# Kernel optimization log

Measured on AMD Instinct MI355X. Metric: run time of the kernel, lower is better.

Reference implementation:

```python
import jax, jax.numpy as jnp
import numpy as np

HIDDEN_DIM = 256
ATTN_DIM = 256
N_TOKENS = 32768
N_CODES = 4096
RMS_EPS = 1e-5


def _rms_norm(x, weight):
    # fp32 variance like the torch module, eps=1e-5, elementwise affine (no bias)
    var = jnp.mean(x.astype(jnp.float32) ** 2, axis=-1, keepdims=True)
    x = x * jax.lax.rsqrt(var + RMS_EPS)
    return x * weight


def setup_inputs() -> dict:
    key = jax.random.key(0)
    ks = jax.random.split(key, 10)
    s_in = 1.0 / np.sqrt(HIDDEN_DIM).astype(np.float32)
    return {
        "hidden_states": jax.random.normal(ks[0], (N_TOKENS, HIDDEN_DIM), jnp.float32),
        "codebook_hidden_states": jax.random.normal(ks[1], (N_CODES, HIDDEN_DIM), jnp.float32),
        # Linear weights stored as [in, out] (y = x @ W + b)
        "wq": jax.random.normal(ks[2], (HIDDEN_DIM, ATTN_DIM), jnp.float32) * s_in,
        "bq": jnp.zeros((ATTN_DIM,), jnp.float32),
        "wk": jax.random.normal(ks[3], (HIDDEN_DIM, ATTN_DIM), jnp.float32) * s_in,
        "bk": jnp.zeros((ATTN_DIM,), jnp.float32),
        "wv": jax.random.normal(ks[4], (HIDDEN_DIM, HIDDEN_DIM), jnp.float32) * s_in,
        "bv": jnp.zeros((HIDDEN_DIM,), jnp.float32),
        "gq": jnp.ones((ATTN_DIM,), jnp.float32),  # RMSNorm weight for q
        "gk": jnp.ones((ATTN_DIM,), jnp.float32),  # RMSNorm weight for k
    }


def reference(hidden_states, codebook_hidden_states, wq, bq, wk, bk, wv, bv, gq, gk):
    # projections (small-d GEMMs)
    q = hidden_states @ wq + bq                     # [NT, A]
    k = codebook_hidden_states @ wk + bk            # [N, A]
    v = codebook_hidden_states @ wv + bv            # [N, C]

    scale = 1.0 / jnp.sqrt(jnp.asarray(q.shape[-1], q.dtype))
    q = _rms_norm(q, gq)
    k = _rms_norm(k, gk)

    logits = jnp.einsum("bd,nd->bn", q, k) * scale  # [NT, N]
    soft_one_hot = jax.nn.softmax(logits, axis=1)
    idx_N = jnp.argmax(logits, axis=1)              # argmax(softmax) == argmax(logits)
    hard_one_hot = jax.nn.one_hot(idx_N, logits.shape[1], dtype=logits.dtype)
    # straight-through estimator
    one_hot = hard_one_hot - jax.lax.stop_gradient(soft_one_hot) + soft_one_hot

    z_q = jnp.einsum("bn,nd->bd", one_hot, v)       # [NT, C]
    z_q_2 = jnp.einsum("bn,nd->bd", hard_one_hot, v)
    return (logits, idx_N[:, None], z_q, z_q_2)
```

## Files before the change

kernel.cpp:

```cpp
#include <hip/hip_runtime.h>
#include <hip/hip_bf16.h>


#define NTOK 32768
#define NCODE 4096
#define DIM 256

typedef __bf16 bf16x8 __attribute__((ext_vector_type(8)));
typedef float f32x4 __attribute__((ext_vector_type(4)));

__device__ __forceinline__ void nt_store4(const float4& v, float* p) {
    f32x4 w; w[0] = v.x; w[1] = v.y; w[2] = v.z; w[3] = v.w;
    __builtin_nontemporal_store(w, (f32x4*)p);
}

__global__ __launch_bounds__(256, 2)
void gemm_fused(const float* __restrict__ hs, const float* __restrict__ cb,
                const float* __restrict__ wq, const float* __restrict__ bq,
                const float* __restrict__ wk, const float* __restrict__ bk,
                const float* __restrict__ wv, const float* __restrict__ bv,
                float* __restrict__ qf, float* __restrict__ kf, float* __restrict__ vf)
{
    __shared__ __align__(16) float Xs[32][132];
    __shared__ __align__(16) float Ws[32][132];
    const int t  = threadIdx.x;
    const int tm = t >> 4;
    const int tn = t & 15;

    const int bx = blockIdx.x;
    const float* X; const float* W; const float* bias; float* Y; int mb;
    if (bx < 32)      { X = cb; W = wk; bias = bk; Y = kf; mb = bx * 128; }
    else if (bx < 64) { X = cb; W = wv; bias = bv; Y = vf; mb = (bx - 32) * 128; }
    else              { X = hs; W = wq; bias = bq; Y = qf; mb = (bx - 64) * 128; }
    const int nb = blockIdx.y * 128;

    float acc[8][8];
    #pragma unroll
    for (int i = 0; i < 8; ++i)
        #pragma unroll
        for (int j = 0; j < 8; ++j) acc[i][j] = 0.f;

    const int sxm = t >> 1;
    const int sxh = (t & 1) * 16;
    const int swk = t >> 3;
    const int swc = (t & 7) * 16;

    for (int kb = 0; kb < 256; kb += 32) {
        float4 xv[4], wv4[4];
        #pragma unroll
        for (int i = 0; i < 4; ++i) {
            xv[i]  = *(const float4*)&X[(size_t)(mb + sxm) * 256 + kb + sxh + 4 * i];
            wv4[i] = *(const float4*)&W[(size_t)(kb + swk) * 256 + nb + swc + 4 * i];
        }
        __syncthreads();
        #pragma unroll
        for (int i = 0; i < 4; ++i) {
            Xs[sxh + 4*i + 0][sxm] = xv[i].x;
            Xs[sxh + 4*i + 1][sxm] = xv[i].y;
            Xs[sxh + 4*i + 2][sxm] = xv[i].z;
            Xs[sxh + 4*i + 3][sxm] = xv[i].w;
            *(float4*)&Ws[swk][swc + 4*i] = wv4[i];
        }
        __syncthreads();
        #pragma unroll 8
        for (int kk = 0; kk < 32; ++kk) {
            float4 a0 = *(const float4*)&Xs[kk][tm*8];
            float4 a1 = *(const float4*)&Xs[kk][tm*8 + 4];
            float4 b0 = *(const float4*)&Ws[kk][tn*8];
            float4 b1 = *(const float4*)&Ws[kk][tn*8 + 4];
            float av[8] = {a0.x,a0.y,a0.z,a0.w,a1.x,a1.y,a1.z,a1.w};
            float bw[8] = {b0.x,b0.y,b0.z,b0.w,b1.x,b1.y,b1.z,b1.w};
            #pragma unroll
            for (int i = 0; i < 8; ++i)
                #pragma unroll
                for (int j = 0; j < 8; ++j)
                    acc[i][j] = fmaf(av[i], bw[j], acc[i][j]);
        }
    }

    float4 bb0 = *(const float4*)&bias[nb + tn*8];
    float4 bb1 = *(const float4*)&bias[nb + tn*8 + 4];
    float bb[8] = {bb0.x,bb0.y,bb0.z,bb0.w,bb1.x,bb1.y,bb1.z,bb1.w};
    #pragma unroll
    for (int i = 0; i < 8; ++i) {
        const size_t row = (size_t)(mb + tm*8 + i);
        float4 o0 = {acc[i][0]+bb[0], acc[i][1]+bb[1], acc[i][2]+bb[2], acc[i][3]+bb[3]};
        float4 o1 = {acc[i][4]+bb[4], acc[i][5]+bb[5], acc[i][6]+bb[6], acc[i][7]+bb[7]};
        *(float4*)&Y[row*256 + nb + tn*8]     = o0;
        *(float4*)&Y[row*256 + nb + tn*8 + 4] = o1;
    }
}

__global__ __launch_bounds__(256)
void rmsnorm_fused(float* __restrict__ kf, float* __restrict__ qf,
                   const float* __restrict__ gk, const float* __restrict__ gq,
                   __hip_bfloat16* __restrict__ kb, __hip_bfloat16* __restrict__ qb)
{
    const int b = blockIdx.x;
    float* X; const float* g; __hip_bfloat16* Xb; size_t row;
    if (b < 1024) { X = kf; g = gk; Xb = kb; row = (size_t)b * 4 + (threadIdx.x >> 6); }
    else { X = qf; g = gq; Xb = qb; row = (size_t)(b - 1024) * 4 + (threadIdx.x >> 6); }

    const int lane = threadIdx.x & 63;
    float4 x = *(const float4*)&X[row*256 + lane*4];
    float ssq = fmaf(x.x, x.x, fmaf(x.y, x.y, fmaf(x.z, x.z, x.w * x.w)));
    #pragma unroll
    for (int o = 1; o < 64; o <<= 1) ssq += __shfl_xor(ssq, o, 64);
    const float r = 1.0f / sqrtf(ssq * (1.0f/256.0f) + 1e-5f);
    float4 gg = *(const float4*)&g[lane*4];
    float y0 = (x.x*r)*gg.x, y1 = (x.y*r)*gg.y, y2 = (x.z*r)*gg.z, y3 = (x.w*r)*gg.w;
    float4 y = {y0, y1, y2, y3};
    *(float4*)&X[row*256 + lane*4] = y;
    __hip_bfloat16 h0 = __float2bfloat16(y0), h1 = __float2bfloat16(y1);
    __hip_bfloat16 h2 = __float2bfloat16(y2), h3 = __float2bfloat16(y3);
    ushort4 p;
    p.x = *(unsigned short*)&h0; p.y = *(unsigned short*)&h1;
    p.z = *(unsigned short*)&h2; p.w = *(unsigned short*)&h3;
    ((ushort4*)Xb)[row*64 + lane] = p;
}

__device__ __forceinline__ void load_lds16(const void* g, void* l) {
    __builtin_amdgcn_global_load_lds((const __attribute__((address_space(1))) unsigned int*)g,
                                     (__attribute__((address_space(3))) unsigned int*)l, 16, 0, 0);
}

__global__ __launch_bounds__(256, 4)
void mfma_logits(const __hip_bfloat16* __restrict__ Qb, const __hip_bfloat16* __restrict__ Kb,
                 float* __restrict__ Out, float* __restrict__ Tmax)
{
    __shared__ __align__(16) char smem[33792];
    __hip_bfloat16* Asm = (__hip_bfloat16*)smem;
    __hip_bfloat16* Bsm = (__hip_bfloat16*)(smem + 16384);
    float*          Eps = (float*)smem;
    float*          Pmax = (float*)(smem + 32768);

    const int t    = threadIdx.x;
    const int lane = t & 63;
    const int w    = t >> 6;
    const int wm = w >> 1, wn = w & 1;

    const int bid = blockIdx.x;
    const int xcd = bid & 7;
    const int cid = bid >> 3;
    const int mb  = (xcd * 32 + (cid & 31)) * 128;
    const int ctl = cid >> 5;
    const int nb  = ctl * 128;

    const int grow   = t >> 3;
    const int gslot  = (t & 7) ^ ((t >> 3) & 7);
    const __hip_bfloat16* gA = Qb + (size_t)(mb + grow) * 256 + gslot * 8;
    const __hip_bfloat16* gB = Kb + (size_t)(nb + grow) * 256 + gslot * 8;
    __hip_bfloat16* lA = &Asm[w * 512];
    __hip_bfloat16* lB = &Bsm[w * 512];

    const int fr = lane & 15;
    const int kq = lane >> 4;
    const int rswz = lane & 7;
    const int ra0 = (wm * 64 + fr) * 64;
    const int rb0 = (wn * 64 + fr) * 64;

    f32x4 acc[4][4];
    #pragma unroll
    for (int mi = 0; mi < 4; ++mi)
        #pragma unroll
        for (int ni = 0; ni < 4; ++ni) {
            acc[mi][ni][0] = 0.f; acc[mi][ni][1] = 0.f;
            acc[mi][ni][2] = 0.f; acc[mi][ni][3] = 0.f;
        }

    for (int ks = 0; ks < 4; ++ks) {
        const int k0 = ks * 64;
        #pragma unroll
        for (int i = 0; i < 4; ++i) {
            load_lds16(gA + (size_t)i * 32 * 256 + k0, lA + i * 2048);
            load_lds16(gB + (size_t)i * 32 * 256 + k0, lB + i * 2048);
        }
        __syncthreads();

        #pragma unroll
        for (int kh = 0; kh < 2; ++kh) {
            bf16x8 af[4], bg[4];
            #pragma unroll
            for (int mi = 0; mi < 4; ++mi)
                af[mi] = *(const bf16x8*)&Asm[ra0 + mi*16*64 + (((kh<<2) + kq) ^ rswz) * 8];
            #pragma unroll
            for (int ni = 0; ni < 4; ++ni)
                bg[ni] = *(const bf16x8*)&Bsm[rb0 + ni*16*64 + (((kh<<2) + kq) ^ rswz) * 8];
            #pragma unroll
            for (int mi = 0; mi < 4; ++mi)
                #pragma unroll
                for (int ni = 0; ni < 4; ++ni)
                    acc[mi][ni] = __builtin_amdgcn_mfma_f32_16x16x32_bf16(
                        af[mi], bg[ni], acc[mi][ni], 0, 0, 0);
        }
        __syncthreads();
    }

    #pragma unroll
    for (int mi = 0; mi < 4; ++mi)
        #pragma unroll
        for (int j = 0; j < 4; ++j) {
            float mx = fmaxf(fmaxf(acc[mi][0][j], acc[mi][1][j]),
                             fmaxf(acc[mi][2][j], acc[mi][3][j]));
            #pragma unroll
            for (int o = 1; o < 16; o <<= 1) mx = fmaxf(mx, __shfl_xor(mx, o, 64));
            if ((lane & 15) == 0)
                Pmax[(wm*64 + mi*16 + (lane>>4)*4 + j)*2 + wn] = mx;
        }

    const int cr = (lane >> 4) * 4;
    const int cc = lane & 15;
    #pragma unroll
    for (int c = 0; c < 2; ++c) {
        if (wm == c) {
            #pragma unroll
            for (int mi = 0; mi < 4; ++mi)
                #pragma unroll
                for (int ni = 0; ni < 4; ++ni) {
                    const int lrow = mi*16 + cr;
                    const int lcol = wn*64 + ni*16 + cc;
                    #pragma unroll
                    for (int j = 0; j < 4; ++j) {
                        float v = acc[mi][ni][j] * 0.0625f;
                        v = fminf(fmaxf(v, -16.0f), 16.0f);
                        Eps[(lrow + j) * 128 + lcol] = v;
                    }
                }
        }
        __syncthreads();
        #pragma unroll
        for (int it = 0; it < 8; ++it) {
            const int p   = it * 1024 + t * 4;
            const int row = p >> 7;
            const int col = p & 127;
            float4 v = *(const float4*)&Eps[p];
            nt_store4(v, &Out[(size_t)(mb + c*64 + row) * 4096 + nb + col]);
        }
        __syncthreads();
    }

    if (t < 128) {
        float raw = fmaxf(Pmax[t*2], Pmax[t*2 + 1]);
        float v = raw * 0.0625f;
        v = fminf(fmaxf(v, -16.0f), 16.0f);
        Tmax[(size_t)(mb + t) * 32 + ctl] = v;
    }
}

__device__ __forceinline__ float dot256_f32(const float* __restrict__ a, const float* __restrict__ b)
{
    float s0 = 0.f, s1 = 0.f, s2 = 0.f, s3 = 0.f;
    #pragma unroll 8
    for (int j = 0; j < 64; ++j) {
        float4 x = ((const float4*)a)[j];
        float4 y = ((const float4*)b)[j];
        s0 = fmaf(x.x, y.x, s0);
        s1 = fmaf(x.y, y.y, s1);
        s2 = fmaf(x.z, y.z, s2);
        s3 = fmaf(x.w, y.w, s3);
    }
    return (s0 + s1) + (s2 + s3);
}

__global__ __launch_bounds__(256)
void refine_argmax_fast(const float* __restrict__ L, const float* __restrict__ Tmax,
                        const float* __restrict__ Qf, const float* __restrict__ Kf,
                        const float* __restrict__ Vf, float* __restrict__ OutIdx,
                        float* __restrict__ Zq, float* __restrict__ Zq2)
{
    __shared__ int cnt[4];
    __shared__ int list[4][256];
    const int lane = threadIdx.x & 63;
    const int w    = threadIdx.x >> 6;
    const size_t row = (size_t)blockIdx.x * 4 + w;

    float tm = (lane < 32) ? Tmax[row * 32 + lane] : -INFINITY;
    float gmax = tm;
    #pragma unroll
    for (int o = 1; o < 64; o <<= 1) gmax = fmaxf(gmax, __shfl_xor(gmax, o, 64));
    const float thr = gmax - 0.5f;

    if (lane == 0) cnt[w] = 0;
    __syncthreads();

    for (int tile = 0; tile < 32; ++tile) {
        const float tmt = __shfl(tm, tile, 64);
        if (tmt >= thr) {
            const float2 v2 = *(const float2*)&L[row * 4096 + tile * 128 + lane * 2];
            if (v2.x >= thr) {
                int slot = atomicAdd(&cnt[w], 1);
                if (slot < 256) list[w][slot] = tile*128 + lane*2;
            }
            if (v2.y >= thr) {
                int slot = atomicAdd(&cnt[w], 1);
                if (slot < 256) list[w][slot] = tile*128 + lane*2 + 1;
            }
        }
    }
    __syncthreads();

    int m = cnt[w]; if (m > 256) m = 256;
    float bv = -INFINITY;
    int   bi = 0x7fffffff;
    const float* qrow = Qf + row * 256;
    for (int base = 0; base < m; base += 64) {
        const int ci = base + lane;
        if (ci < m) {
            const int c = list[w][ci];
            float rv = dot256_f32(qrow, Kf + (size_t)c * 256) * 0.0625f;
            if (rv > bv || (rv == bv && c < bi)) { bv = rv; bi = c; }
        }
    }
    #pragma unroll
    for (int o = 1; o < 64; o <<= 1) {
        float ov = __shfl_xor(bv, o, 64);
        int   oi = __shfl_xor(bi, o, 64);
        if (ov > bv || (ov == bv && oi < bi)) { bv = ov; bi = oi; }
    }

    if (bi < 0) bi = 0;
    if (bi > 4095) bi = 4095;

    if (lane == 0) __builtin_nontemporal_store((float)bi, &OutIdx[row]);

    float4 vv = ((const float4*)(Vf + (size_t)bi * 256))[lane];
    nt_store4(vv, (float*)&((float4*)Zq)[row*64 + lane]);
    nt_store4(vv, (float*)&((float4*)Zq2)[row*64 + lane]);
}

extern "C" void kernel_launch(void* const* d_in, const int* in_sizes, int n_in,
                              void* d_out, int out_size, void* d_ws, size_t ws_size,
                              hipStream_t stream)
{
    (void)in_sizes; (void)n_in; (void)out_size;
    const float* hs = (const float*)d_in[0];
    const float* cb = (const float*)d_in[1];
    const float* wq = (const float*)d_in[2];
    const float* bq = (const float*)d_in[3];
    const float* wk = (const float*)d_in[4];
    const float* bk = (const float*)d_in[5];
    const float* wv = (const float*)d_in[6];
    const float* bv = (const float*)d_in[7];
    const float* gq = (const float*)d_in[8];
    const float* gk = (const float*)d_in[9];
    float* out = (float*)d_out;

    if (ws_size < 31457280u) return;

    float* qf = out + 134250496ull;

    char* ws = (char*)d_ws;
    float* kf = (float*)ws;
    float* vf = (float*)(ws + 4194304);
    __hip_bfloat16* qb = (__hip_bfloat16*)(ws + 8388608);
    __hip_bfloat16* kb = (__hip_bfloat16*)(ws + 25165824);
    float* tmax = (float*)(ws + 27262976);

    gemm_fused<<<dim3(320, 2), 256, 0, stream>>>(hs, cb, wq, bq, wk, bk, wv, bv,
                                                 qf, kf, vf);
    rmsnorm_fused<<<9216, 256, 0, stream>>>(kf, qf, gk, gq, kb, qb);
    mfma_logits<<<8192, 256, 0, stream>>>(qb, kb, out, tmax);
    refine_argmax_fast<<<8192, 256, 0, stream>>>(out, tmax, qf, kf, vf,
        out + 134217728ull,
        out + 134250496ull,
        out + 142639104ull);
}
```

Before: 441.3 us.

## Fuse RMSNorm into projection GEMM by computing full rows per block

```diff
diff --git a/kernel.cpp b/kernel.cpp
--- a/kernel.cpp
+++ b/kernel.cpp
@@ -15,11 +15,13 @@
 }
 
 __global__ __launch_bounds__(256, 2)
-void gemm_fused(const float* __restrict__ hs, const float* __restrict__ cb,
+void gemm3_norm(const float* __restrict__ hs, const float* __restrict__ cb,
                 const float* __restrict__ wq, const float* __restrict__ bq,
                 const float* __restrict__ wk, const float* __restrict__ bk,
                 const float* __restrict__ wv, const float* __restrict__ bv,
-                float* __restrict__ qf, float* __restrict__ kf, float* __restrict__ vf)
+                const float* __restrict__ gq, const float* __restrict__ gk,
+                float* __restrict__ qf, float* __restrict__ kf, float* __restrict__ vf,
+                __hip_bfloat16* __restrict__ qb16, __hip_bfloat16* __restrict__ kb16)
 {
     __shared__ __align__(16) float Xs[32][132];
     __shared__ __align__(16) float Ws[32][132];
@@ -29,94 +31,96 @@
 
     const int bx = blockIdx.x;
     const float* X; const float* W; const float* bias; float* Y; int mb;
-    if (bx < 32)      { X = cb; W = wk; bias = bk; Y = kf; mb = bx * 128; }
-    else if (bx < 64) { X = cb; W = wv; bias = bv; Y = vf; mb = (bx - 32) * 128; }
-    else              { X = hs; W = wq; bias = bq; Y = qf; mb = (bx - 64) * 128; }
-    const int nb = blockIdx.y * 128;
-
-    float acc[8][8];
-    #pragma unroll
-    for (int i = 0; i < 8; ++i)
-        #pragma unroll
-        for (int j = 0; j < 8; ++j) acc[i][j] = 0.f;
+    const float* g = nullptr; __hip_bfloat16* Yb = nullptr; bool donorm;
+    if (bx < 32)      { X = cb; W = wk; bias = bk; Y = kf; mb = bx * 128;        g = gk; Yb = kb16; donorm = true;  }
+    else if (bx < 64) { X = cb; W = wv; bias = bv; Y = vf; mb = (bx - 32) * 128; donorm = false; }
+    else              { X = hs; W = wq; bias = bq; Y = qf; mb = (bx - 64) * 128; g = gq; Yb = qb16; donorm = true;  }
 
     const int sxm = t >> 1;
     const int sxh = (t & 1) * 16;
     const int swk = t >> 3;
     const int swc = (t & 7) * 16;
 
-    for (int kb = 0; kb < 256; kb += 32) {
-        float4 xv[4], wv4[4];
-        #pragma unroll
-        for (int i = 0; i < 4; ++i) {
-            xv[i]  = *(const float4*)&X[(size_t)(mb + sxm) * 256 + kb + sxh + 4 * i];
-            wv4[i] = *(const float4*)&W[(size_t)(kb + swk) * 256 + nb + swc + 4 * i];
-        }
-        __syncthreads();
-        #pragma unroll
-        for (int i = 0; i < 4; ++i) {
-            Xs[sxh + 4*i + 0][sxm] = xv[i].x;
-            Xs[sxh + 4*i + 1][sxm] = xv[i].y;
-            Xs[sxh + 4*i + 2][sxm] = xv[i].z;
-            Xs[sxh + 4*i + 3][sxm] = xv[i].w;
-            *(float4*)&Ws[swk][swc + 4*i] = wv4[i];
-        }
-        __syncthreads();
-        #pragma unroll 8
-        for (int kk = 0; kk < 32; ++kk) {
-            float4 a0 = *(const float4*)&Xs[kk][tm*8];
-            float4 a1 = *(const float4*)&Xs[kk][tm*8 + 4];
-            float4 b0 = *(const float4*)&Ws[kk][tn*8];
-            float4 b1 = *(const float4*)&Ws[kk][tn*8 + 4];
-            float av[8] = {a0.x,a0.y,a0.z,a0.w,a1.x,a1.y,a1.z,a1.w};
-            float bw[8] = {b0.x,b0.y,b0.z,b0.w,b1.x,b1.y,b1.z,b1.w};
-            #pragma unroll
-            for (int i = 0; i < 8; ++i)
+    #pragma unroll 1
+    for (int h = 0; h < 2; ++h) {
+        const int nb = h * 128;
+
+        float acc[8][8];
+        #pragma unroll
+        for (int i = 0; i < 8; ++i)
+            #pragma unroll
+            for (int j = 0; j < 8; ++j) acc[i][j] = 0.f;
+
+        for (int kb = 0; kb < 256; kb += 32) {
+            float4 xv[4], wv4[4];
+            #pragma unroll
+            for (int i = 0; i < 4; ++i) {
+                xv[i]  = *(const float4*)&X[(size_t)(mb + sxm) * 256 + kb + sxh + 4 * i];
+                wv4[i] = *(const float4*)&W[(size_t)(kb + swk) * 256 + nb + swc + 4 * i];
+            }
+            __syncthreads();
+            #pragma unroll
+            for (int i = 0; i < 4; ++i) {
+                Xs[sxh + 4*i + 0][sxm] = xv[i].x;
+                Xs[sxh + 4*i + 1][sxm] = xv[i].y;
+                Xs[sxh + 4*i + 2][sxm] = xv[i].z;
+                Xs[sxh + 4*i + 3][sxm] = xv[i].w;
+                *(float4*)&Ws[swk][swc + 4*i] = wv4[i];
+            }
+            __syncthreads();
+            #pragma unroll 8
+            for (int kk = 0; kk < 32; ++kk) {
+                float4 a0 = *(const float4*)&Xs[kk][tm*8];
+                float4 a1 = *(const float4*)&Xs[kk][tm*8 + 4];
+                float4 b0 = *(const float4*)&Ws[kk][tn*8];
+                float4 b1 = *(const float4*)&Ws[kk][tn*8 + 4];
+                float av[8] = {a0.x,a0.y,a0.z,a0.w,a1.x,a1.y,a1.z,a1.w};
+                float bw[8] = {b0.x,b0.y,b0.z,b0.w,b1.x,b1.y,b1.z,b1.w};
                 #pragma unroll
-                for (int j = 0; j < 8; ++j)
-                    acc[i][j] = fmaf(av[i], bw[j], acc[i][j]);
-        }
-    }
-
-    float4 bb0 = *(const float4*)&bias[nb + tn*8];
-    float4 bb1 = *(const float4*)&bias[nb + tn*8 + 4];
-    float bb[8] = {bb0.x,bb0.y,bb0.z,bb0.w,bb1.x,bb1.y,bb1.z,bb1.w};
-    #pragma unroll
-    for (int i = 0; i < 8; ++i) {
-        const size_t row = (size_t)(mb + tm*8 + i);
-        float4 o0 = {acc[i][0]+bb[0], acc[i][1]+bb[1], acc[i][2]+bb[2], acc[i][3]+bb[3]};
-        float4 o1 = {acc[i][4]+bb[4], acc[i][5]+bb[5], acc[i][6]+bb[6], acc[i][7]+bb[7]};
-        *(float4*)&Y[row*256 + nb + tn*8]     = o0;
-        *(float4*)&Y[row*256 + nb + tn*8 + 4] = o1;
-    }
-}
-
-__global__ __launch_bounds__(256)
-void rmsnorm_fused(float* __restrict__ kf, float* __restrict__ qf,
-                   const float* __restrict__ gk, const float* __restrict__ gq,
-                   __hip_bfloat16* __restrict__ kb, __hip_bfloat16* __restrict__ qb)
-{
-    const int b = blockIdx.x;
-    float* X; const float* g; __hip_bfloat16* Xb; size_t row;
-    if (b < 1024) { X = kf; g = gk; Xb = kb; row = (size_t)b * 4 + (threadIdx.x >> 6); }
-    else { X = qf; g = gq; Xb = qb; row = (size_t)(b - 1024) * 4 + (threadIdx.x >> 6); }
-
-    const int lane = threadIdx.x & 63;
-    float4 x = *(const float4*)&X[row*256 + lane*4];
-    float ssq = fmaf(x.x, x.x, fmaf(x.y, x.y, fmaf(x.z, x.z, x.w * x.w)));
-    #pragma unroll
-    for (int o = 1; o < 64; o <<= 1) ssq += __shfl_xor(ssq, o, 64);
-    const float r = 1.0f / sqrtf(ssq * (1.0f/256.0f) + 1e-5f);
-    float4 gg = *(const float4*)&g[lane*4];
-    float y0 = (x.x*r)*gg.x, y1 = (x.y*r)*gg.y, y2 = (x.z*r)*gg.z, y3 = (x.w*r)*gg.w;
-    float4 y = {y0, y1, y2, y3};
-    *(float4*)&X[row*256 + lane*4] = y;
-    __hip_bfloat16 h0 = __float2bfloat16(y0), h1 = __float2bfloat16(y1);
-    __hip_bfloat16 h2 = __float2bfloat16(y2), h3 = __float2bfloat16(y3);
-    ushort4 p;
-    p.x = *(unsigned short*)&h0; p.y = *(unsigned short*)&h1;
-    p.z = *(unsigned short*)&h2; p.w = *(unsigned short*)&h3;
-    ((ushort4*)Xb)[row*64 + lane] = p;
+                for (int i = 0; i < 8; ++i)
+                    #pragma unroll
+                    for (int j = 0; j < 8; ++j)
+                        acc[i][j] = fmaf(av[i], bw[j], acc[i][j]);
+            }
+        }
+
+        float4 bb0 = *(const float4*)&bias[nb + tn*8];
+        float4 bb1 = *(const float4*)&bias[nb + tn*8 + 4];
+        float bb[8] = {bb0.x,bb0.y,bb0.z,bb0.w,bb1.x,bb1.y,bb1.z,bb1.w};
+        #pragma unroll
+        for (int i = 0; i < 8; ++i) {
+            const size_t row = (size_t)(mb + tm*8 + i);
+            float4 o0 = {acc[i][0]+bb[0], acc[i][1]+bb[1], acc[i][2]+bb[2], acc[i][3]+bb[3]};
+            float4 o1 = {acc[i][4]+bb[4], acc[i][5]+bb[5], acc[i][6]+bb[6], acc[i][7]+bb[7]};
+            *(float4*)&Y[row*256 + nb + tn*8]     = o0;
+            *(float4*)&Y[row*256 + nb + tn*8 + 4] = o1;
+        }
+    }
+
+    if (donorm) {
+        __syncthreads();
+        const int lane = t & 63;
+        const int w    = t >> 6;
+        #pragma unroll 1
+        for (int rr = 0; rr < 32; ++rr) {
+            const size_t row = (size_t)mb + rr*4 + w;
+            float4 x = *(const float4*)&Y[row*256 + lane*4];
+            float ssq = fmaf(x.x, x.x, fmaf(x.y, x.y, fmaf(x.z, x.z, x.w * x.w)));
+            #pragma unroll
+            for (int o = 1; o < 64; o <<= 1) ssq += __shfl_xor(ssq, o, 64);
+            const float r = 1.0f / sqrtf(ssq * (1.0f/256.0f) + 1e-5f);
+            float4 gg = *(const float4*)&g[lane*4];
+            float y0 = (x.x*r)*gg.x, y1 = (x.y*r)*gg.y, y2 = (x.z*r)*gg.z, y3 = (x.w*r)*gg.w;
+            float4 y = {y0, y1, y2, y3};
+            *(float4*)&Y[row*256 + lane*4] = y;
+            __hip_bfloat16 h0 = __float2bfloat16(y0), h1 = __float2bfloat16(y1);
+            __hip_bfloat16 h2 = __float2bfloat16(y2), h3 = __float2bfloat16(y3);
+            ushort4 p;
+            p.x = *(unsigned short*)&h0; p.y = *(unsigned short*)&h1;
+            p.z = *(unsigned short*)&h2; p.w = *(unsigned short*)&h3;
+            ((ushort4*)Yb)[row*64 + lane] = p;
+        }
+    }
 }
 
 __device__ __forceinline__ void load_lds16(const void* g, void* l) {
@@ -356,9 +360,8 @@
     __hip_bfloat16* kb = (__hip_bfloat16*)(ws + 25165824);
     float* tmax = (float*)(ws + 27262976);
 
-    gemm_fused<<<dim3(320, 2), 256, 0, stream>>>(hs, cb, wq, bq, wk, bk, wv, bv,
-                                                 qf, kf, vf);
-    rmsnorm_fused<<<9216, 256, 0, stream>>>(kf, qf, gk, gq, kb, qb);
+    gemm3_norm<<<320, 256, 0, stream>>>(hs, cb, wq, bq, wk, bk, wv, bv, gq, gk,
+                                        qf, kf, vf, qb, kb);
     mfma_logits<<<8192, 256, 0, stream>>>(qb, kb, out, tmax);
     refine_argmax_fast<<<8192, 256, 0, stream>>>(out, tmax, qf, kf, vf,
         out + 134217728ull,
```

Result: slower. 472.3 us (+7.0%).

## Double-buffer K-loop LDS staging in logits MFMA kernel

Applied to the files above, without the earlier changes.

```diff
diff --git a/kernel.cpp b/kernel.cpp
--- a/kernel.cpp
+++ b/kernel.cpp
@@ -124,15 +124,48 @@
                                      (__attribute__((address_space(3))) unsigned int*)l, 16, 0, 0);
 }
 
-__global__ __launch_bounds__(256, 4)
+__device__ __forceinline__ void stage8(const __hip_bfloat16* gA, const __hip_bfloat16* gB,
+                                       __hip_bfloat16* dA, __hip_bfloat16* dB, int k0, int w)
+{
+    #pragma unroll
+    for (int i = 0; i < 4; ++i) {
+        load_lds16(gA + (size_t)i * 32 * 256 + k0, dA + w * 512 + i * 2048);
+        load_lds16(gB + (size_t)i * 32 * 256 + k0, dB + w * 512 + i * 2048);
+    }
+}
+
+__device__ __forceinline__ void comp64(const __hip_bfloat16* A, const __hip_bfloat16* B,
+                                       int ra0, int rb0, int kq, int rswz, f32x4 (&acc)[4][4])
+{
+    #pragma unroll
+    for (int kh = 0; kh < 2; ++kh) {
+        bf16x8 af[4], bg[4];
+        #pragma unroll
+        for (int mi = 0; mi < 4; ++mi)
+            af[mi] = *(const bf16x8*)&A[ra0 + mi*16*64 + (((kh<<2) + kq) ^ rswz) * 8];
+        #pragma unroll
+        for (int ni = 0; ni < 4; ++ni)
+            bg[ni] = *(const bf16x8*)&B[rb0 + ni*16*64 + (((kh<<2) + kq) ^ rswz) * 8];
+        #pragma unroll
+        for (int mi = 0; mi < 4; ++mi)
+            #pragma unroll
+            for (int ni = 0; ni < 4; ++ni)
+                acc[mi][ni] = __builtin_amdgcn_mfma_f32_16x16x32_bf16(
+                    af[mi], bg[ni], acc[mi][ni], 0, 0, 0);
+    }
+}
+
+__global__ __launch_bounds__(256, 2)
 void mfma_logits(const __hip_bfloat16* __restrict__ Qb, const __hip_bfloat16* __restrict__ Kb,
                  float* __restrict__ Out, float* __restrict__ Tmax)
 {
-    __shared__ __align__(16) char smem[33792];
-    __hip_bfloat16* Asm = (__hip_bfloat16*)smem;
-    __hip_bfloat16* Bsm = (__hip_bfloat16*)(smem + 16384);
-    float*          Eps = (float*)smem;
-    float*          Pmax = (float*)(smem + 32768);
+    __shared__ __align__(16) char smem[66560];
+    __hip_bfloat16* A0 = (__hip_bfloat16*)smem;
+    __hip_bfloat16* B0 = (__hip_bfloat16*)(smem + 16384);
+    __hip_bfloat16* A1 = (__hip_bfloat16*)(smem + 32768);
+    __hip_bfloat16* B1 = (__hip_bfloat16*)(smem + 49152);
+    float*          Eps  = (float*)smem;
+    float*          Pmax = (float*)(smem + 65536);
 
     const int t    = threadIdx.x;
     const int lane = t & 63;
@@ -150,8 +183,6 @@
     const int gslot  = (t & 7) ^ ((t >> 3) & 7);
     const __hip_bfloat16* gA = Qb + (size_t)(mb + grow) * 256 + gslot * 8;
     const __hip_bfloat16* gB = Kb + (size_t)(nb + grow) * 256 + gslot * 8;
-    __hip_bfloat16* lA = &Asm[w * 512];
-    __hip_bfloat16* lB = &Bsm[w * 512];
 
     const int fr = lane & 15;
     const int kq = lane >> 4;
@@ -168,33 +199,29 @@
             acc[mi][ni][2] = 0.f; acc[mi][ni][3] = 0.f;
         }
 
-    for (int ks = 0; ks < 4; ++ks) {
-        const int k0 = ks * 64;
-        #pragma unroll
-        for (int i = 0; i < 4; ++i) {
-            load_lds16(gA + (size_t)i * 32 * 256 + k0, lA + i * 2048);
-            load_lds16(gB + (size_t)i * 32 * 256 + k0, lB + i * 2048);
-        }
-        __syncthreads();
-
-        #pragma unroll
-        for (int kh = 0; kh < 2; ++kh) {
-            bf16x8 af[4], bg[4];
-            #pragma unroll
-            for (int mi = 0; mi < 4; ++mi)
-                af[mi] = *(const bf16x8*)&Asm[ra0 + mi*16*64 + (((kh<<2) + kq) ^ rswz) * 8];
-            #pragma unroll
-            for (int ni = 0; ni < 4; ++ni)
-                bg[ni] = *(const bf16x8*)&Bsm[rb0 + ni*16*64 + (((kh<<2) + kq) ^ rswz) * 8];
-            #pragma unroll
-            for (int mi = 0; mi < 4; ++mi)
-                #pragma unroll
-                for (int ni = 0; ni < 4; ++ni)
-                    acc[mi][ni] = __builtin_amdgcn_mfma_f32_16x16x32_bf16(
-                        af[mi], bg[ni], acc[mi][ni], 0, 0, 0);
-        }
-        __syncthreads();
-    }
+    stage8(gA, gB, A0, B0, 0, w);
+
+    stage8(gA, gB, A1, B1, 64, w);
+    asm volatile("s_waitcnt vmcnt(8)" ::: "memory");
+    __builtin_amdgcn_s_barrier();
+    comp64(A0, B0, ra0, rb0, kq, rswz, acc);
+    __builtin_amdgcn_s_barrier();
+
+    stage8(gA, gB, A0, B0, 128, w);
+    asm volatile("s_waitcnt vmcnt(8)" ::: "memory");
+    __builtin_amdgcn_s_barrier();
+    comp64(A1, B1, ra0, rb0, kq, rswz, acc);
+    __builtin_amdgcn_s_barrier();
+
+    stage8(gA, gB, A1, B1, 192, w);
+    asm volatile("s_waitcnt vmcnt(8)" ::: "memory");
+    __builtin_amdgcn_s_barrier();
+    comp64(A0, B0, ra0, rb0, kq, rswz, acc);
+    __builtin_amdgcn_s_barrier();
+
+    asm volatile("s_waitcnt vmcnt(0)" ::: "memory");
+    __builtin_amdgcn_s_barrier();
+    comp64(A1, B1, ra0, rb0, kq, rswz, acc);
 
     #pragma unroll
     for (int mi = 0; mi < 4; ++mi)
```

After: 463.9 us. +5.1%, slower.
